# Kernel tuning notes

Measured on AMD Instinct MI355X. Metric: run time of the kernel, lower is better.

The kernel has to match this reference:

```python
import jax, jax.numpy as jnp
import numpy as np

N_NODES = 100000
N_EDGES = 1600000
IN_DIM = 128
HID = 64
OUT_DIM = 1


def setup_inputs() -> dict:
    key = jax.random.key(0)
    ks = jax.random.split(key, 8)
    x = jax.random.normal(ks[0], (N_NODES, IN_DIM), dtype=jnp.float32)
    edge_index = jax.random.randint(ks[1], (2, N_EDGES), 0, N_NODES, dtype=jnp.int64)
    s_in = 1.0 / np.sqrt(IN_DIM)
    s_h = 1.0 / np.sqrt(HID)
    W_in = jax.random.uniform(ks[2], (IN_DIM, HID), jnp.float32, -s_in, s_in)
    b_in = jax.random.uniform(ks[3], (HID,), jnp.float32, -s_in, s_in)
    W_g = jax.random.uniform(ks[4], (HID, HID), jnp.float32, -s_h, s_h)
    b_g = jnp.zeros((HID,), jnp.float32)
    W_out = jax.random.uniform(ks[5], (HID, OUT_DIM), jnp.float32, -s_h, s_h)
    b_out = jax.random.uniform(ks[6], (OUT_DIM,), jnp.float32, -s_h, s_h)
    return {"x": x, "edge_index": edge_index, "W_in": W_in, "b_in": b_in,
            "W_g": W_g, "b_g": b_g, "W_out": W_out, "b_out": b_out}


def _gcn_conv(h, src, dst, W, b, n_nodes):
    # GCNConv: add self-loops, symmetric normalization, sum aggregation
    loops = jnp.arange(n_nodes, dtype=src.dtype)
    src = jnp.concatenate([src, loops])
    dst = jnp.concatenate([dst, loops])
    hw = h @ W  # [N, out]
    deg = jax.ops.segment_sum(jnp.ones_like(dst, dtype=hw.dtype), dst,
                              num_segments=n_nodes)  # >=1 due to self-loops
    dinv = jax.lax.rsqrt(deg)
    norm = dinv[src] * dinv[dst]  # [E+N]
    msg = hw[src] * norm[:, None]  # gather (memory-bound)
    out = jax.ops.segment_sum(msg, dst, num_segments=n_nodes)  # scatter-add
    return out + b


def reference(x, edge_index, W_in, b_in, W_g, b_g, W_out, b_out):
    n_nodes = x.shape[0]
    h = jax.nn.relu(x @ W_in + b_in)  # input_proj + ReLU (dropout = id in eval)
    # single GCN layer (last layer -> no ReLU/dropout after)
    h = _gcn_conv(h, edge_index[0], edge_index[1], W_g, b_g, n_nodes)
    return h @ W_out + b_out  # [N, 1]
```

## Files before the change

### kernel.cpp

```cpp
#include <hip/hip_runtime.h>

typedef __attribute__((ext_vector_type(8))) short bf16x8;
typedef __attribute__((ext_vector_type(4))) float f32x4;

#define HID 64
#define IN_DIM 128
#define RANGE_BITS 14
#define RANGE (1 << RANGE_BITS)
#define NB 7
#define MCH 36
#define SCAN_TPB 512
#define RB2 15
#define RANGE2 (1 << RB2)
#define NB2 4
#define MCH2 64
#define DNODES 64
#define LDSXP 136

__device__ __forceinline__ unsigned short f2bf(float f) {
    unsigned u = __builtin_bit_cast(unsigned, f);
    return (unsigned short)((u + 0x7FFFu + ((u >> 16) & 1u)) >> 16);
}

__global__ __launch_bounds__(256) void k_prep(const float* __restrict__ W_in,
                                              unsigned short* __restrict__ Wt) {
    int i = blockIdx.x * 256 + threadIdx.x;
    if (i < IN_DIM * HID) {
        int j = i >> 7, k = i & 127;
        Wt[i] = f2bf(W_in[k * HID + j]);
    }
}

__global__ __launch_bounds__(256) void k_dense(const float* __restrict__ x,
                                               const unsigned short* __restrict__ Wt,
                                               const float* __restrict__ b_in,
                                               const float* __restrict__ W_g,
                                               const float* __restrict__ W_out,
                                               const unsigned* __restrict__ partA,
                                               float* __restrict__ dinv,
                                               float* __restrict__ zs,
                                               int N) {
    __shared__ float weff_l[HID];
    __shared__ float bl[HID];
    __shared__ unsigned short ldsX[DNODES * LDSXP];
    __shared__ float zp[DNODES];

    const int t = threadIdx.x;
    const int row0 = blockIdx.x * DNODES;

    float4 rg[8];
    const int lrow = t >> 3;
    const int lcol = (t & 7) * 4;
    {
        int gr0 = row0 + lrow;        if (gr0 >= N) gr0 = N - 1;
        int gr1 = row0 + 32 + lrow;   if (gr1 >= N) gr1 = N - 1;
        const float* p0 = x + (size_t)gr0 * IN_DIM + lcol;
        const float* p1 = x + (size_t)gr1 * IN_DIM + lcol;
#pragma unroll
        for (int c = 0; c < 4; ++c) {
            rg[c * 2 + 0] = *(const float4*)(p0 + c * 32);
            rg[c * 2 + 1] = *(const float4*)(p1 + c * 32);
        }
    }

    {
        const float* wg = W_g + (t >> 2) * HID + (t & 3) * 16;
        const float* wo = W_out + (t & 3) * 16;
        float s = 0.0f;
#pragma unroll
        for (int p = 0; p < 16; ++p) s = fmaf(wg[p], wo[p], s);
        s += __shfl_xor(s, 1, 64);
        s += __shfl_xor(s, 2, 64);
        if ((t & 3) == 0) weff_l[t >> 2] = s;
        if (t < HID) bl[t] = b_in[t];
    }

    const int w    = __builtin_amdgcn_readfirstlane(t >> 6);
    const int lane = t & 63;

    bf16x8 bfr[4][4];
    {
        const int col = lane & 15;
        const int ko  = (lane >> 4) * 8;
#pragma unroll
        for (int nf = 0; nf < 4; ++nf)
#pragma unroll
            for (int kk = 0; kk < 4; ++kk)
                bfr[nf][kk] = *(const bf16x8*)(Wt + (size_t)(nf * 16 + col) * IN_DIM + kk * 32 + ko);
    }

#pragma unroll
    for (int c = 0; c < 4; ++c) {
        float4 v0 = rg[c * 2 + 0], v1 = rg[c * 2 + 1];
        ushort4 h0 = { f2bf(v0.x), f2bf(v0.y), f2bf(v0.z), f2bf(v0.w) };
        ushort4 h1 = { f2bf(v1.x), f2bf(v1.y), f2bf(v1.z), f2bf(v1.w) };
        *(ushort4*)&ldsX[lrow * LDSXP + c * 32 + lcol]        = h0;
        *(ushort4*)&ldsX[(32 + lrow) * LDSXP + c * 32 + lcol] = h1;
    }
    __syncthreads();

    f32x4 acc[4] = {{0,0,0,0},{0,0,0,0},{0,0,0,0},{0,0,0,0}};
    {
        const int arow = w * 16 + (lane & 15);
        const int ko   = (lane >> 4) * 8;
#pragma unroll
        for (int kk = 0; kk < 4; ++kk) {
            bf16x8 af = *(const bf16x8*)&ldsX[arow * LDSXP + kk * 32 + ko];
#pragma unroll
            for (int nf = 0; nf < 4; ++nf)
                acc[nf] = __builtin_amdgcn_mfma_f32_16x16x32_bf16(af, bfr[nf][kk], acc[nf], 0, 0, 0);
        }
    }

    {
        float p[4] = {0.f, 0.f, 0.f, 0.f};
#pragma unroll
        for (int nf = 0; nf < 4; ++nf) {
            const int col = nf * 16 + (lane & 15);
            const float bc = bl[col], wc = weff_l[col];
#pragma unroll
            for (int r = 0; r < 4; ++r)
                p[r] = fmaf(fmaxf(acc[nf][r] + bc, 0.0f), wc, p[r]);
        }
#pragma unroll
        for (int r = 0; r < 4; ++r) {
            p[r] += __shfl_xor(p[r], 1, 64);
            p[r] += __shfl_xor(p[r], 2, 64);
            p[r] += __shfl_xor(p[r], 4, 64);
            p[r] += __shfl_xor(p[r], 8, 64);
        }
        if ((lane & 15) == 0) {
#pragma unroll
            for (int r = 0; r < 4; ++r)
                zp[w * 16 + (lane >> 4) * 4 + r] = p[r];
        }
    }
    __syncthreads();

    if (t < 64) {
        int n = row0 + t; if (n >= N) n = N - 1;
        float z = zp[t];
        const int r = n >> RB2, idx = n & (RANGE2 - 1);
        const int sh = (idx & 1) << 4;
        const unsigned* base = partA + (size_t)r * (RANGE2 / 2) + (idx >> 1);
        const size_t stride = (size_t)NB2 * (RANGE2 / 2);
        int d = 0;
#pragma unroll 8
        for (int m = 0; m < MCH2; ++m)
            d += (int)((base[m * stride] >> sh) & 0xFFFFu);
        float di = rsqrtf((float)d + 1.0f);
        dinv[n] = di;
        zs[n]   = z * di;
    }
}

__global__ __launch_bounds__(SCAN_TPB) void k_binA(const int* __restrict__ dst,
                                                   unsigned* __restrict__ partA,
                                                   int E, int chunkA) {
    __shared__ unsigned cnt[RANGE2 / 2];
    for (int i = threadIdx.x; i < RANGE2 / 2; i += SCAN_TPB) cnt[i] = 0;
    __syncthreads();

    const int r = blockIdx.x % NB2;
    const int lo = r << RB2;
    const int e0 = (blockIdx.x / NB2) * chunkA;
    const int e1 = min(E, e0 + chunkA);
    for (int e = e0 + (int)threadIdx.x * 4; e + 3 < e1; e += SCAN_TPB * 4) {
        int4 d4 = *(const int4*)(dst + e);
        unsigned v;
        v = (unsigned)(d4.x - lo); if (v < RANGE2) atomicAdd(&cnt[v >> 1], 1u << ((v & 1) << 4));
        v = (unsigned)(d4.y - lo); if (v < RANGE2) atomicAdd(&cnt[v >> 1], 1u << ((v & 1) << 4));
        v = (unsigned)(d4.z - lo); if (v < RANGE2) atomicAdd(&cnt[v >> 1], 1u << ((v & 1) << 4));
        v = (unsigned)(d4.w - lo); if (v < RANGE2) atomicAdd(&cnt[v >> 1], 1u << ((v & 1) << 4));
    }
    __syncthreads();

    unsigned* outp = partA + (size_t)blockIdx.x * (RANGE2 / 2);
    for (int i = threadIdx.x; i < RANGE2 / 2; i += SCAN_TPB) outp[i] = cnt[i];
}

__global__ __launch_bounds__(SCAN_TPB) void k_binC(const int* __restrict__ eidx,
                                                   const float* __restrict__ zs,
                                                   float* __restrict__ partf,
                                                   int E, int chunk) {
    __shared__ float acc[RANGE];
    for (int i = threadIdx.x; i < RANGE; i += SCAN_TPB) acc[i] = 0.0f;
    __syncthreads();

    const int r = blockIdx.x % NB;
    const int lo = r << RANGE_BITS;
    const int e0 = (blockIdx.x / NB) * chunk;
    const int e1 = min(E, e0 + chunk);
    for (int e = e0 + (int)threadIdx.x * 4; e + 3 < e1; e += SCAN_TPB * 4) {
        int4 s4 = *(const int4*)(eidx + e);
        int4 d4 = *(const int4*)(eidx + E + e);
        unsigned v;
        v = (unsigned)(d4.x - lo); if (v < RANGE) atomicAdd(&acc[v], zs[s4.x]);
        v = (unsigned)(d4.y - lo); if (v < RANGE) atomicAdd(&acc[v], zs[s4.y]);
        v = (unsigned)(d4.z - lo); if (v < RANGE) atomicAdd(&acc[v], zs[s4.z]);
        v = (unsigned)(d4.w - lo); if (v < RANGE) atomicAdd(&acc[v], zs[s4.w]);
    }
    __syncthreads();

    float* outp = partf + (size_t)blockIdx.x * RANGE;
    for (int i = threadIdx.x; i < RANGE; i += SCAN_TPB) outp[i] = acc[i];
}

__global__ __launch_bounds__(256) void k_redFinal(const float* __restrict__ partf,
                                                  const float* __restrict__ dinv,
                                                  const float* __restrict__ zs,
                                                  const float* __restrict__ b_g,
                                                  const float* __restrict__ W_out,
                                                  const float* __restrict__ b_out,
                                                  float* __restrict__ out, int N) {
    const int lane = threadIdx.x & 63;
    float c = b_g[lane] * W_out[lane];
#pragma unroll
    for (int off = 32; off > 0; off >>= 1)
        c += __shfl_xor(c, off, 64);
    c += b_out[0];

    int i = blockIdx.x * blockDim.x + threadIdx.x;
    if (i >= N) return;
    const int r = i >> RANGE_BITS, idx = i & (RANGE - 1);
    float a = zs[i];
#pragma unroll 4
    for (int m = 0; m < MCH; ++m)
        a += partf[((size_t)m * NB + r) * RANGE + idx];
    out[i] = fmaf(dinv[i], a, c);
}


extern "C" void kernel_launch(void* const* d_in, const int* in_sizes, int n_in,
                              void* d_out, int out_size, void* d_ws, size_t ws_size,
                              hipStream_t stream) {
    const float* x     = (const float*)d_in[0];
    const int*   eidx  = (const int*)d_in[1];
    const float* W_in  = (const float*)d_in[2];
    const float* b_in  = (const float*)d_in[3];
    const float* W_g   = (const float*)d_in[4];
    const float* b_g   = (const float*)d_in[5];
    const float* W_out = (const float*)d_in[6];
    const float* b_out = (const float*)d_in[7];
    float* out = (float*)d_out;

    const int N = in_sizes[0] / IN_DIM;
    const int E = in_sizes[1] / 2;

    const int chunk  = (((E + MCH  - 1) / MCH ) + 3) & ~3;
    const int chunkA = (((E + MCH2 - 1) / MCH2) + 3) & ~3;

    const size_t partElems0 = (size_t)NB * MCH * RANGE;
    const size_t partElemsA = (size_t)NB2 * MCH2 * (RANGE2 / 2);
    const size_t partElems = partElems0 > partElemsA ? partElems0 : partElemsA;
    unsigned* partA = (unsigned*)d_ws;
    float*    partf = (float*)d_ws;
    float*    dinv  = (float*)d_ws + partElems;
    float*    zs    = dinv + N;
    unsigned short* Wt = (unsigned short*)(zs + N);

    const int nG = (N + DNODES - 1) / DNODES;
    k_prep<<<(IN_DIM * HID + 255) / 256, 256, 0, stream>>>(W_in, Wt);
    k_binA<<<NB2 * MCH2, SCAN_TPB, 0, stream>>>(eidx + E, partA, E, chunkA);
    k_dense<<<nG, 256, 0, stream>>>(x, Wt, b_in, W_g, W_out, partA, dinv, zs, N);
    k_binC<<<NB * MCH, SCAN_TPB, 0, stream>>>(eidx, zs, partf, E, chunk);
    k_redFinal<<<(N + 255) / 256, 256, 0, stream>>>(partf, dinv, zs, b_g, W_out, b_out, out, N);
}
```

Before: 81.80 us.

## Fuse weight prep into binA, load x directly into MFMA fragments, split degree reduction

The weight transpose/bf16 conversion is folded into extra blocks of the degree-binning kernel, which removes one launch. The dense kernel now reads x straight from global memory into MFMA A fragments and drops the LDS staging buffer and its barrier. The 64-chunk degree sum is split across all 4 waves with an LDS reduction instead of running on one wave. In exchange, the direct x loads are narrower and less coalesced than the old float4 row loads, so memory efficiency may drop.

```diff
diff --git a/kernel.cpp b/kernel.cpp
--- a/kernel.cpp
+++ b/kernel.cpp
@@ -14,21 +14,45 @@
 #define RANGE2 (1 << RB2)
 #define NB2 4
 #define MCH2 64
+#define PREP_BLOCKS 16
 #define DNODES 64
-#define LDSXP 136
 
 __device__ __forceinline__ unsigned short f2bf(float f) {
     unsigned u = __builtin_bit_cast(unsigned, f);
     return (unsigned short)((u + 0x7FFFu + ((u >> 16) & 1u)) >> 16);
 }
 
-__global__ __launch_bounds__(256) void k_prep(const float* __restrict__ W_in,
-                                              unsigned short* __restrict__ Wt) {
-    int i = blockIdx.x * 256 + threadIdx.x;
-    if (i < IN_DIM * HID) {
-        int j = i >> 7, k = i & 127;
-        Wt[i] = f2bf(W_in[k * HID + j]);
-    }
+__global__ __launch_bounds__(SCAN_TPB) void k_binA(const int* __restrict__ dst,
+                                                   unsigned* __restrict__ partA,
+                                                   const float* __restrict__ W_in,
+                                                   unsigned short* __restrict__ Wt,
+                                                   int E, int chunkA) {
+    if ((int)blockIdx.x >= NB2 * MCH2) {
+        int i = (blockIdx.x - NB2 * MCH2) * SCAN_TPB + threadIdx.x;
+        if (i < IN_DIM * HID) Wt[i] = f2bf(W_in[(i & 127) * HID + (i >> 7)]);
+        return;
+    }
+
+    __shared__ unsigned cnt[RANGE2 / 2];
+    for (int i = threadIdx.x; i < RANGE2 / 2; i += SCAN_TPB) cnt[i] = 0;
+    __syncthreads();
+
+    const int r = blockIdx.x % NB2;
+    const int lo = r << RB2;
+    const int e0 = (blockIdx.x / NB2) * chunkA;
+    const int e1 = min(E, e0 + chunkA);
+    for (int e = e0 + (int)threadIdx.x * 4; e + 3 < e1; e += SCAN_TPB * 4) {
+        int4 d4 = *(const int4*)(dst + e);
+        unsigned v;
+        v = (unsigned)(d4.x - lo); if (v < RANGE2) atomicAdd(&cnt[v >> 1], 1u << ((v & 1) << 4));
+        v = (unsigned)(d4.y - lo); if (v < RANGE2) atomicAdd(&cnt[v >> 1], 1u << ((v & 1) << 4));
+        v = (unsigned)(d4.z - lo); if (v < RANGE2) atomicAdd(&cnt[v >> 1], 1u << ((v & 1) << 4));
+        v = (unsigned)(d4.w - lo); if (v < RANGE2) atomicAdd(&cnt[v >> 1], 1u << ((v & 1) << 4));
+    }
+    __syncthreads();
+
+    unsigned* outp = partA + (size_t)blockIdx.x * (RANGE2 / 2);
+    for (int i = threadIdx.x; i < RANGE2 / 2; i += SCAN_TPB) outp[i] = cnt[i];
 }
 
 __global__ __launch_bounds__(256) void k_dense(const float* __restrict__ x,
@@ -42,26 +66,11 @@
                                                int N) {
     __shared__ float weff_l[HID];
     __shared__ float bl[HID];
-    __shared__ unsigned short ldsX[DNODES * LDSXP];
     __shared__ float zp[DNODES];
+    __shared__ int   tailp[4][DNODES];
 
     const int t = threadIdx.x;
     const int row0 = blockIdx.x * DNODES;
-
-    float4 rg[8];
-    const int lrow = t >> 3;
-    const int lcol = (t & 7) * 4;
-    {
-        int gr0 = row0 + lrow;        if (gr0 >= N) gr0 = N - 1;
-        int gr1 = row0 + 32 + lrow;   if (gr1 >= N) gr1 = N - 1;
-        const float* p0 = x + (size_t)gr0 * IN_DIM + lcol;
-        const float* p1 = x + (size_t)gr1 * IN_DIM + lcol;
-#pragma unroll
-        for (int c = 0; c < 4; ++c) {
-            rg[c * 2 + 0] = *(const float4*)(p0 + c * 32);
-            rg[c * 2 + 1] = *(const float4*)(p1 + c * 32);
-        }
-    }
 
     {
         const float* wg = W_g + (t >> 2) * HID + (t & 3) * 16;
@@ -89,28 +98,26 @@
                 bfr[nf][kk] = *(const bf16x8*)(Wt + (size_t)(nf * 16 + col) * IN_DIM + kk * 32 + ko);
     }
 
-#pragma unroll
-    for (int c = 0; c < 4; ++c) {
-        float4 v0 = rg[c * 2 + 0], v1 = rg[c * 2 + 1];
-        ushort4 h0 = { f2bf(v0.x), f2bf(v0.y), f2bf(v0.z), f2bf(v0.w) };
-        ushort4 h1 = { f2bf(v1.x), f2bf(v1.y), f2bf(v1.z), f2bf(v1.w) };
-        *(ushort4*)&ldsX[lrow * LDSXP + c * 32 + lcol]        = h0;
-        *(ushort4*)&ldsX[(32 + lrow) * LDSXP + c * 32 + lcol] = h1;
-    }
-    __syncthreads();
-
     f32x4 acc[4] = {{0,0,0,0},{0,0,0,0},{0,0,0,0},{0,0,0,0}};
     {
-        const int arow = w * 16 + (lane & 15);
-        const int ko   = (lane >> 4) * 8;
+        int grow = row0 + w * 16 + (lane & 15);
+        if (grow >= N) grow = N - 1;
+        const float* xr = x + (size_t)grow * IN_DIM + (lane >> 4) * 8;
 #pragma unroll
         for (int kk = 0; kk < 4; ++kk) {
-            bf16x8 af = *(const bf16x8*)&ldsX[arow * LDSXP + kk * 32 + ko];
+            float4 a0 = *(const float4*)(xr + kk * 32);
+            float4 a1 = *(const float4*)(xr + kk * 32 + 4);
+            bf16x8 af;
+            af[0] = (short)f2bf(a0.x); af[1] = (short)f2bf(a0.y);
+            af[2] = (short)f2bf(a0.z); af[3] = (short)f2bf(a0.w);
+            af[4] = (short)f2bf(a1.x); af[5] = (short)f2bf(a1.y);
+            af[6] = (short)f2bf(a1.z); af[7] = (short)f2bf(a1.w);
 #pragma unroll
             for (int nf = 0; nf < 4; ++nf)
                 acc[nf] = __builtin_amdgcn_mfma_f32_16x16x32_bf16(af, bfr[nf][kk], acc[nf], 0, 0, 0);
         }
     }
+    __syncthreads();
 
     {
         float p[4] = {0.f, 0.f, 0.f, 0.f};
@@ -135,48 +142,30 @@
                 zp[w * 16 + (lane >> 4) * 4 + r] = p[r];
         }
     }
-    __syncthreads();
-
-    if (t < 64) {
-        int n = row0 + t; if (n >= N) n = N - 1;
-        float z = zp[t];
+
+    {
+        const int tn = t & 63;
+        const int tq = t >> 6;
+        int n = row0 + tn; if (n >= N) n = N - 1;
         const int r = n >> RB2, idx = n & (RANGE2 - 1);
         const int sh = (idx & 1) << 4;
         const unsigned* base = partA + (size_t)r * (RANGE2 / 2) + (idx >> 1);
         const size_t stride = (size_t)NB2 * (RANGE2 / 2);
         int d = 0;
-#pragma unroll 8
-        for (int m = 0; m < MCH2; ++m)
-            d += (int)((base[m * stride] >> sh) & 0xFFFFu);
+#pragma unroll
+        for (int j = 0; j < 16; ++j)
+            d += (int)((base[(size_t)(tq * 16 + j) * stride] >> sh) & 0xFFFFu);
+        tailp[tq][tn] = d;
+    }
+    __syncthreads();
+
+    if (t < 64) {
+        int n = row0 + t; if (n >= N) n = N - 1;
+        int d = tailp[0][t] + tailp[1][t] + tailp[2][t] + tailp[3][t];
         float di = rsqrtf((float)d + 1.0f);
         dinv[n] = di;
-        zs[n]   = z * di;
-    }
-}
-
-__global__ __launch_bounds__(SCAN_TPB) void k_binA(const int* __restrict__ dst,
-                                                   unsigned* __restrict__ partA,
-                                                   int E, int chunkA) {
-    __shared__ unsigned cnt[RANGE2 / 2];
-    for (int i = threadIdx.x; i < RANGE2 / 2; i += SCAN_TPB) cnt[i] = 0;
-    __syncthreads();
-
-    const int r = blockIdx.x % NB2;
-    const int lo = r << RB2;
-    const int e0 = (blockIdx.x / NB2) * chunkA;
-    const int e1 = min(E, e0 + chunkA);
-    for (int e = e0 + (int)threadIdx.x * 4; e + 3 < e1; e += SCAN_TPB * 4) {
-        int4 d4 = *(const int4*)(dst + e);
-        unsigned v;
-        v = (unsigned)(d4.x - lo); if (v < RANGE2) atomicAdd(&cnt[v >> 1], 1u << ((v & 1) << 4));
-        v = (unsigned)(d4.y - lo); if (v < RANGE2) atomicAdd(&cnt[v >> 1], 1u << ((v & 1) << 4));
-        v = (unsigned)(d4.z - lo); if (v < RANGE2) atomicAdd(&cnt[v >> 1], 1u << ((v & 1) << 4));
-        v = (unsigned)(d4.w - lo); if (v < RANGE2) atomicAdd(&cnt[v >> 1], 1u << ((v & 1) << 4));
-    }
-    __syncthreads();
-
-    unsigned* outp = partA + (size_t)blockIdx.x * (RANGE2 / 2);
-    for (int i = threadIdx.x; i < RANGE2 / 2; i += SCAN_TPB) outp[i] = cnt[i];
+        zs[n]   = zp[t] * di;
+    }
 }
 
 __global__ __launch_bounds__(SCAN_TPB) void k_binC(const int* __restrict__ eidx,
@@ -260,8 +249,7 @@
     unsigned short* Wt = (unsigned short*)(zs + N);
 
     const int nG = (N + DNODES - 1) / DNODES;
-    k_prep<<<(IN_DIM * HID + 255) / 256, 256, 0, stream>>>(W_in, Wt);
-    k_binA<<<NB2 * MCH2, SCAN_TPB, 0, stream>>>(eidx + E, partA, E, chunkA);
+    k_binA<<<NB2 * MCH2 + PREP_BLOCKS, SCAN_TPB, 0, stream>>>(eidx + E, partA, W_in, Wt, E, chunkA);
     k_dense<<<nG, 256, 0, stream>>>(x, Wt, b_in, W_g, W_out, partA, dinv, zs, N);
     k_binC<<<NB * MCH, SCAN_TPB, 0, stream>>>(eidx, zs, partf, E, chunk);
     k_redFinal<<<(N + 255) / 256, 256, 0, stream>>>(partf, dinv, zs, b_g, W_out, b_out, out, N);
```

After: 79.47 us. 2.8% less time.
